# Performance work log

Hardware: AMD Instinct MI355X
Metric: run time of the kernel (lower is better)

The kernel has to match this reference:

```python
import jax, jax.numpy as jnp
import numpy as np

B, C, H, W, K = 8, 128, 128, 128, 7


def _ln2d(x, gamma=None, beta=None, eps=1e-5):
    # LayerNorm2d: normalize over the channel dim at each (b, h, w) position
    mu = x.mean(axis=1, keepdims=True)
    var = x.var(axis=1, keepdims=True)
    y = (x - mu) * jax.lax.rsqrt(var + eps)
    if gamma is not None:
        y = y * gamma[None, :, None, None] + beta[None, :, None, None]
    return y


def _conv1x1(x, w, b):
    # w: [C_out, C_in] (1x1 conv collapsed)
    return jnp.einsum('oi,bihw->bohw', w, x) + b[None, :, None, None]


def _sym_conv(x, w):
    # channel-symmetric 7x7 conv, padding 'same' (SymmetricConv2d, symmetry_type='channel')
    ws = 0.5 * (w + jnp.swapaxes(w, 0, 1))
    return jax.lax.conv_general_dilated(
        x, ws, window_strides=(1, 1), padding='SAME',
        dimension_numbers=('NCHW', 'OIHW', 'NCHW'))


def setup_inputs() -> dict:
    key = jax.random.key(0)
    ks = jax.random.split(key, 8)
    f32 = jnp.float32
    return {
        'ff_input': jax.random.normal(ks[0], (B, C, H, W), f32),
        'h_exc': jax.random.normal(ks[1], (B, C, H, W), f32),
        'h_inh': jax.random.normal(ks[2], (B, C, H, W), f32),
        # 1x1 gate convs over concat([h_exc, h_inh, ff]) -> C channels
        'W_gain': jax.random.normal(ks[3], (C, 3 * C), f32) * 0.02,
        'b_gain': jnp.zeros((C,), f32),
        'W_mix': jax.random.normal(ks[4], (C, 3 * C), f32) * 0.02,
        'b_mix': jnp.zeros((C,), f32),
        # symmetric 7x7 horizontal connections
        'W_inh': jax.random.normal(ks[5], (C, C, K, K), f32) * 0.01,
        'W_exc': jax.random.normal(ks[6], (C, C, K, K), f32) * 0.01,
        # static circuit parameters (use_dynamic_parameters=False)
        'alpha': jnp.zeros((C,), f32),
        'mu': jnp.zeros((C,), f32),
        'kappa': jnp.ones((C,), f32) * 0.1,
        'omega': jnp.ones((C,), f32) * 0.1,
        # affine LayerNorm2d for circuit outputs c1/c2
        'c1_gamma': jnp.ones((C,), f32), 'c1_beta': jnp.zeros((C,), f32),
        'c2_gamma': jnp.ones((C,), f32), 'c2_beta': jnp.zeros((C,), f32),
    }


def reference(ff_input, h_exc, h_inh, W_gain, b_gain, W_mix, b_mix,
              W_inh, W_exc, alpha, mu, kappa, omega,
              c1_gamma, c1_beta, c2_gamma, c2_beta):
    # --- stage 1: gain gate (pre-norm on concat, 1x1 conv, sigmoid) ---
    g1_in = _ln2d(jnp.concatenate([h_exc, h_inh, ff_input], axis=1))  # [B,3C,H,W]
    g1 = jax.nn.sigmoid(_conv1x1(g1_in, W_gain, b_gain))              # [B,C,H,W]

    # --- stage 2: horizontal inhibition from gain-controlled excitatory state ---
    c1 = _ln2d(_sym_conv(h_exc * g1, W_inh), c1_gamma, c1_beta)

    # --- stage 3: input integration: divisive (alpha) + subtractive (mu) inhibition ---
    a = jax.nn.sigmoid(alpha)[None, :, None, None]  # force_alpha_divisive
    m = mu[None, :, None, None]
    inhibited = jax.nn.relu(ff_input - jax.nn.relu((a * h_inh + m) * c1))

    # --- stage 4: mix gate ---
    g2_in = _ln2d(jnp.concatenate([inhibited, h_exc, h_inh], axis=1))
    g2 = jax.nn.sigmoid(_conv1x1(g2_in, W_mix, b_mix))

    # --- stage 5: excitatory horizontal connections ---
    c2 = _ln2d(_sym_conv(inhibited, W_exc), c2_gamma, c2_beta)

    # --- stage 6: output integration (multiplicative excitation) ---
    k = kappa[None, :, None, None]
    o = jax.nn.relu(omega)[None, :, None, None]  # force_omega_nonnegative
    h_tilde = jax.nn.relu(k * (inhibited + c2) + o * (inhibited * c2))

    # --- gated state update of the excitatory population ---
    h_exc_new = (1.0 - g2) * h_exc + g2 * h_tilde
    return h_exc_new
```

## Files before the change

kernel.cpp:

```cpp
#include <hip/hip_runtime.h>
#include <cstddef>
#include <cstdint>

namespace {
constexpr int B_ = 8, C_ = 128, H_ = 128, W_ = 128;
constexpr int HW_ = H_ * W_;
constexpr size_t CHW_ = (size_t)C_ * HW_;
constexpr int NPIX_ = B_ * HW_;
}

typedef __attribute__((ext_vector_type(8))) short bf16x8;
typedef __attribute__((ext_vector_type(4))) float f32x4;
typedef __attribute__((ext_vector_type(8))) unsigned short u16x8;
typedef __attribute__((ext_vector_type(4))) unsigned short u16x4;

__device__ inline unsigned short f2bf(float f) {
  unsigned int u = __float_as_uint(f);
  unsigned int r = u + 0x7FFFu + ((u >> 16) & 1u);
  return (unsigned short)(r >> 16);
}
__device__ inline float bf2f(unsigned short u) {
  return __uint_as_float((unsigned int)u << 16);
}

__device__ inline void async_copy16(void* lds_dst, const void* gsrc) {
  __builtin_amdgcn_global_load_lds(
      (const __attribute__((address_space(1))) unsigned int*)gsrc,
      (__attribute__((address_space(3))) unsigned int*)lds_dst, 16, 0, 0);
}

__global__ __launch_bounds__(256) void prep_w_bf16_k(
    const float* __restrict__ Wa, const float* __restrict__ Wb,
    unsigned short* __restrict__ Ta, unsigned short* __restrict__ Tb) {
  int idx = blockIdx.x * 256 + threadIdx.x;
  int j = idx & 7;
  int o = (idx >> 3) & 127;
  int g = (idx >> 10) & 15;
  int t = idx >> 14;
  int i = g * 8 + j;
  int ky = t / 7, kx = t - ky * 7;
  size_t oi = ((size_t)(o * 128 + i) * 7 + ky) * 7 + kx;
  size_t io = ((size_t)(i * 128 + o) * 7 + ky) * 7 + kx;
  Ta[idx] = f2bf(0.5f * (Wa[oi] + Wa[io]));
  Tb[idx] = f2bf(0.5f * (Wb[oi] + Wb[io]));
}

__global__ __launch_bounds__(256) void prep_apack_k(
    const float* __restrict__ Wg, const float* __restrict__ Wm,
    unsigned short* __restrict__ Ag, unsigned short* __restrict__ Am) {
  int idx = blockIdx.x * 256 + threadIdx.x;
  int j = idx & 7;
  int l = (idx >> 3) & 63;
  int f = (idx >> 9) & 7;
  int s = idx >> 12;
  int m = f * 16 + (l & 15);
  int k = s * 32 + (l >> 4) * 8 + j;
  Ag[idx] = f2bf(Wg[m * 384 + k]);
  Am[idx] = f2bf(Wm[m * 384 + k]);
}

__global__ void rowsum_k(const float* __restrict__ Wg,
                         const float* __restrict__ Wm, float* __restrict__ rs) {
  int t = threadIdx.x;
  const float* src = (t < 128) ? Wg : Wm;
  int row = t & 127;
  float s = 0.f;
  for (int i = 0; i < 384; ++i) s += bf2f(f2bf(src[row * 384 + i]));
  rs[t] = s;
}

__global__ __launch_bounds__(256) void stats3_cvt_k(
    const float* __restrict__ t0, const float* __restrict__ t1,
    const float* __restrict__ t2, float* __restrict__ mu_o,
    float* __restrict__ inv_o, float* __restrict__ ps12,
    float* __restrict__ pq12, unsigned short* __restrict__ o0,
    unsigned short* __restrict__ o1, unsigned short* __restrict__ o2) {
  __shared__ unsigned short tile[32 * 136];
  __shared__ float s8[8][32];
  __shared__ float q8[8][32];
  int blk = blockIdx.x;
  int b = blk >> 9;
  int p0 = (blk & 511) * 32;
  int t = threadIdx.x;
  int px = t & 31, cq = t >> 5;
  size_t base = (size_t)b * CHW_ + p0 + px;
  int pixg = b * HW_ + p0;
  float s = 0.f, s2 = 0.f;
  for (int ci = 0; ci < 16; ++ci) {
    int c = cq * 16 + ci;
    float v = t0[base + (size_t)c * HW_];
    s += v; s2 = fmaf(v, v, s2);
    tile[px * 136 + c] = f2bf(v);
  }
  __syncthreads();
#pragma unroll
  for (int pass = 0; pass < 2; ++pass) {
    int u = pass * 256 + t;
    int ppx = u >> 4, cg = u & 15;
    *(u16x8*)(o0 + (size_t)(pixg + ppx) * 128 + cg * 8) =
        *(const u16x8*)(tile + ppx * 136 + cg * 8);
  }
  __syncthreads();
  for (int ci = 0; ci < 16; ++ci) {
    int c = cq * 16 + ci;
    float v = t1[base + (size_t)c * HW_];
    s += v; s2 = fmaf(v, v, s2);
    tile[px * 136 + c] = f2bf(v);
  }
  s8[cq][px] = s;
  q8[cq][px] = s2;
  __syncthreads();
#pragma unroll
  for (int pass = 0; pass < 2; ++pass) {
    int u = pass * 256 + t;
    int ppx = u >> 4, cg = u & 15;
    *(u16x8*)(o1 + (size_t)(pixg + ppx) * 128 + cg * 8) =
        *(const u16x8*)(tile + ppx * 136 + cg * 8);
  }
  if (t < 32) {
    float ss = 0.f, qs = 0.f;
#pragma unroll
    for (int k = 0; k < 8; ++k) { ss += s8[k][t]; qs += q8[k][t]; }
    ps12[pixg + t] = ss;
    pq12[pixg + t] = qs;
  }
  __syncthreads();
  for (int ci = 0; ci < 16; ++ci) {
    int c = cq * 16 + ci;
    float v = t2[base + (size_t)c * HW_];
    s += v; s2 = fmaf(v, v, s2);
    tile[px * 136 + c] = f2bf(v);
  }
  s8[cq][px] = s;
  q8[cq][px] = s2;
  __syncthreads();
#pragma unroll
  for (int pass = 0; pass < 2; ++pass) {
    int u = pass * 256 + t;
    int ppx = u >> 4, cg = u & 15;
    *(u16x8*)(o2 + (size_t)(pixg + ppx) * 128 + cg * 8) =
        *(const u16x8*)(tile + ppx * 136 + cg * 8);
  }
  if (t < 32) {
    float ss = 0.f, qs = 0.f;
#pragma unroll
    for (int k = 0; k < 8; ++k) { ss += s8[k][t]; qs += q8[k][t]; }
    float m = ss * (1.f / 384.f);
    float var = qs * (1.f / 384.f) - m * m;
    mu_o[pixg + t] = m;
    inv_o[pixg + t] = rsqrtf(var + 1e-5f);
  }
}

template <int FINAL>
__global__ __launch_bounds__(256) void gemm_mfma_k(
    const unsigned short* __restrict__ Apack, const float* __restrict__ rowsum,
    const float* __restrict__ bias, const unsigned short* __restrict__ B0,
    const unsigned short* __restrict__ B1, const unsigned short* __restrict__ B2,
    const float* __restrict__ mu, const float* __restrict__ inv,
    const unsigned short* __restrict__ mult_cl, unsigned short* __restrict__ out_cl,
    const unsigned short* __restrict__ c2_cl, const float* __restrict__ muc,
    const float* __restrict__ invc, const unsigned short* __restrict__ inh_cl,
    const unsigned short* __restrict__ hexc_cl, const float* __restrict__ c2g,
    const float* __restrict__ c2b, const float* __restrict__ kap,
    const float* __restrict__ omg, float* __restrict__ out_f32) {
  int b = blockIdx.y;
  int tid = threadIdx.x;
  int lane = tid & 63, wid = tid >> 6;
  int l15 = lane & 15, kg = lane >> 4;
  int n0 = blockIdx.x * 128 + wid * 32;
  int pix0 = b * HW_ + n0;
  size_t bofs = (size_t)b * CHW_;
  f32x4 acc[8][2] = {};
#pragma unroll
  for (int s = 0; s < 12; ++s) {
    const unsigned short* src = (s < 4) ? B0 : ((s < 8) ? B1 : B2);
    int ch0 = (s & 3) * 32 + kg * 8;
    bf16x8 bfr[2];
#pragma unroll
    for (int nf = 0; nf < 2; ++nf)
      bfr[nf] = *(const bf16x8*)(src + (size_t)(pix0 + nf * 16 + l15) * 128 + ch0);
    const bf16x8* ap = (const bf16x8*)(Apack + ((size_t)(s * 8) * 64 + lane) * 8);
#pragma unroll
    for (int f = 0; f < 8; ++f) {
      bf16x8 afr = ap[f * 64];
#pragma unroll
      for (int nf = 0; nf < 2; ++nf)
        acc[f][nf] = __builtin_amdgcn_mfma_f32_16x16x32_bf16(afr, bfr[nf],
                                                             acc[f][nf], 0, 0, 0);
    }
  }
#pragma unroll
  for (int nf = 0; nf < 2; ++nf) {
    int n = n0 + nf * 16 + l15;
    int qpix = b * HW_ + n;
    float muv = mu[qpix], invv = inv[qpix];
    if (!FINAL) {
#pragma unroll
      for (int mf = 0; mf < 8; ++mf) {
        int m0 = mf * 16 + kg * 4;
        f32x4 rs4 = *(const f32x4*)(rowsum + m0);
        f32x4 bi4 = *(const f32x4*)(bias + m0);
        u16x4 mv = *(const u16x4*)(mult_cl + (size_t)qpix * 128 + m0);
        u16x4 st;
#pragma unroll
        for (int j = 0; j < 4; ++j) {
          float val = invv * (acc[mf][nf][j] - muv * rs4[j]) + bi4[j];
          float g = 1.f / (1.f + __expf(-val));
          st[j] = f2bf(bf2f(mv[j]) * g);
        }
        *(u16x4*)(out_cl + (size_t)qpix * 128 + m0) = st;
      }
    } else {
      float mcv = muc[qpix], icv = invc[qpix];
#pragma unroll
      for (int mf = 0; mf < 8; ++mf) {
        int m0 = mf * 16 + kg * 4;
        f32x4 rs4 = *(const f32x4*)(rowsum + m0);
        f32x4 bi4 = *(const f32x4*)(bias + m0);
        f32x4 g4 = *(const f32x4*)(c2g + m0);
        f32x4 b4 = *(const f32x4*)(c2b + m0);
        f32x4 k4 = *(const f32x4*)(kap + m0);
        f32x4 o4 = *(const f32x4*)(omg + m0);
        u16x4 c2v = *(const u16x4*)(c2_cl + (size_t)qpix * 128 + m0);
        u16x4 iv4 = *(const u16x4*)(inh_cl + (size_t)qpix * 128 + m0);
        u16x4 hx4 = *(const u16x4*)(hexc_cl + (size_t)qpix * 128 + m0);
#pragma unroll
        for (int j = 0; j < 4; ++j) {
          float val = invv * (acc[mf][nf][j] - muv * rs4[j]) + bi4[j];
          float g2 = 1.f / (1.f + __expf(-val));
          float c2 = (bf2f(c2v[j]) - mcv) * icv * g4[j] + b4[j];
          float iv = bf2f(iv4[j]);
          float ht =
              fmaxf(k4[j] * (iv + c2) + fmaxf(o4[j], 0.f) * (iv * c2), 0.f);
          out_f32[bofs + (size_t)(m0 + j) * HW_ + n] =
              (1.f - g2) * bf2f(hx4[j]) + g2 * ht;
        }
      }
    }
  }
}

__global__ __launch_bounds__(256, 2) void conv7_mfma_k(
    const unsigned short* __restrict__ in_cl,
    const unsigned short* __restrict__ Wp, unsigned short* __restrict__ out,
    float* __restrict__ mu_o, float* __restrict__ inv_o) {
  __shared__ short w_s[7 * 4 * 128 * 8];
  __shared__ short in_s[2 * 4 * 136 * 8];
  int b = blockIdx.x & 7;
  int y0 = ((blockIdx.x >> 3) & 63) * 2;
  int tid = threadIdx.x;
  int lane = tid & 63;
  int wid = tid >> 6;
  int wm = wid >> 1;
  int row = wid & 1;
  int l15 = lane & 15, kg = lane >> 4;
  f32x4 acc[4][8] = {};
  for (int ky = 0; ky < 7; ++ky) {
    int ybase = y0 + ky - 3;
    for (int c4 = 0; c4 < 4; ++c4) {
      __syncthreads();
      const unsigned short* wsrc =
          Wp + (size_t)(ky * 7) * 16384 + c4 * 4096 + tid * 8;
#pragma unroll
      for (int kx = 0; kx < 7; ++kx) {
#pragma unroll
        for (int h = 0; h < 2; ++h) {
          async_copy16(w_s + kx * 4096 + (h * 256 + tid) * 8,
                       wsrc + kx * 16384 + h * 2048);
        }
      }
      for (int u = tid; u < 1088; u += 256) {
        int r = u / 544;
        int rem = u - r * 544;
        int g = rem / 136;
        int xi = rem - g * 136;
        int x = xi - 3;
        int y = ybase + r;
        u16x8 v = {};
        if (x >= 0 && x < 128 && y >= 0 && y < 128)
          v = *(const u16x8*)(in_cl + ((size_t)((b * 128 + y) * 128 + x) * 128 +
                                       c4 * 32 + g * 8));
        *(u16x8*)(in_s + u * 8) = v;
      }
      __syncthreads();
      for (int kx = 0; kx < 7; ++kx) {
        bf16x8 bfr[8], afr[4];
#pragma unroll
        for (int nf = 0; nf < 8; ++nf) {
          int xi = nf * 16 + l15 + kx;
          bfr[nf] = *(const bf16x8*)(in_s + ((row * 4 + kg) * 136 + xi) * 8);
        }
#pragma unroll
        for (int mf = 0; mf < 4; ++mf) {
          int oc = wm * 64 + mf * 16 + l15;
          afr[mf] = *(const bf16x8*)(w_s + ((kx * 4 + kg) * 128 + oc) * 8);
        }
#pragma unroll
        for (int mf = 0; mf < 4; ++mf)
#pragma unroll
          for (int nf = 0; nf < 8; ++nf)
            acc[mf][nf] = __builtin_amdgcn_mfma_f32_16x16x32_bf16(
                afr[mf], bfr[nf], acc[mf][nf], 0, 0, 0);
      }
    }
  }
  __syncthreads();
  float* red = (float*)in_s;
  int y = y0 + row;
#pragma unroll
  for (int nf = 0; nf < 8; ++nf) {
    int x = nf * 16 + l15;
    size_t paddr = (size_t)(b * HW_ + y * 128 + x) * 128;
    float s = 0.f, qq = 0.f;
#pragma unroll
    for (int mf = 0; mf < 4; ++mf) {
      int oc0 = wm * 64 + mf * 16 + kg * 4;
      u16x4 st;
#pragma unroll
      for (int j = 0; j < 4; ++j) {
        unsigned short bv = f2bf(acc[mf][nf][j]);
        float vr = bf2f(bv);
        s += vr;
        qq = fmaf(vr, vr, qq);
        st[j] = bv;
      }
      *(u16x4*)(out + paddr + oc0) = st;
    }
    s += __shfl_xor(s, 16);
    qq += __shfl_xor(qq, 16);
    s += __shfl_xor(s, 32);
    qq += __shfl_xor(qq, 32);
    if (kg == 0) {
      red[(wm * 2 + row) * 128 + x] = s;
      red[512 + (wm * 2 + row) * 128 + x] = qq;
    }
  }
  __syncthreads();
  {
    int r2 = tid >> 7, x2 = tid & 127;
    float s = red[(0 * 2 + r2) * 128 + x2] + red[(1 * 2 + r2) * 128 + x2];
    float qq = red[512 + (0 * 2 + r2) * 128 + x2] +
               red[512 + (1 * 2 + r2) * 128 + x2];
    float m = s * (1.f / 128.f);
    float var = qq * (1.f / 128.f) - m * m;
    int q = b * HW_ + (y0 + r2) * 128 + x2;
    mu_o[q] = m;
    inv_o[q] = rsqrtf(var + 1e-5f);
  }
}

__global__ __launch_bounds__(256) void inhibit_k(
    const unsigned short* __restrict__ c1_cl,
    unsigned short* __restrict__ ffio_cl,
    const unsigned short* __restrict__ hinh_cl, const float* __restrict__ mu_s,
    const float* __restrict__ inv_s, const float* __restrict__ ps12,
    const float* __restrict__ pq12, const float* __restrict__ alpha,
    const float* __restrict__ mu_p, const float* __restrict__ gamma,
    const float* __restrict__ beta, float* __restrict__ mu2_o,
    float* __restrict__ inv2_o) {
  __shared__ float s16[16][17];
  __shared__ float q16[16][17];
  int blk = blockIdx.x;
  int t = threadIdx.x;
  int cg = t & 15, pxi = t >> 4;
  int pix = blk * 16 + pxi;
  size_t base = (size_t)pix * 128 + cg * 8;
  int c0 = cg * 8;
  float muv = mu_s[pix], invv = inv_s[pix];
  u16x8 c1v = *(const u16x8*)(c1_cl + base);
  u16x8 ffv = *(const u16x8*)(ffio_cl + base);
  u16x8 hiv = *(const u16x8*)(hinh_cl + base);
  f32x4 al0 = *(const f32x4*)(alpha + c0), al1 = *(const f32x4*)(alpha + c0 + 4);
  f32x4 mp0 = *(const f32x4*)(mu_p + c0), mp1 = *(const f32x4*)(mu_p + c0 + 4);
  f32x4 ga0 = *(const f32x4*)(gamma + c0), ga1 = *(const f32x4*)(gamma + c0 + 4);
  f32x4 be0 = *(const f32x4*)(beta + c0), be1 = *(const f32x4*)(beta + c0 + 4);
  float sp = 0.f, qp = 0.f;
  u16x8 ov;
#pragma unroll
  for (int j = 0; j < 8; ++j) {
    float alv = (j < 4) ? al0[j & 3] : al1[j & 3];
    float mpv = (j < 4) ? mp0[j & 3] : mp1[j & 3];
    float gav = (j < 4) ? ga0[j & 3] : ga1[j & 3];
    float bev = (j < 4) ? be0[j & 3] : be1[j & 3];
    float c1 = (bf2f(c1v[j]) - muv) * invv * gav + bev;
    float a = 1.f / (1.f + __expf(-alv));
    float r = fmaxf((a * bf2f(hiv[j]) + mpv) * c1, 0.f);
    float v = fmaxf(bf2f(ffv[j]) - r, 0.f);
    unsigned short bv = f2bf(v);
    float vr = bf2f(bv);
    sp += vr;
    qp = fmaf(vr, vr, qp);
    ov[j] = bv;
  }
  *(u16x8*)(ffio_cl + base) = ov;
  s16[pxi][cg] = sp;
  q16[pxi][cg] = qp;
  __syncthreads();
  if (t < 16) {
    float s = 0.f, qs = 0.f;
#pragma unroll
    for (int k = 0; k < 16; ++k) { s += s16[t][k]; qs += q16[t][k]; }
    int pg = blk * 16 + t;
    s += ps12[pg];
    qs += pq12[pg];
    float m = s * (1.f / 384.f);
    float var = qs * (1.f / 384.f) - m * m;
    mu2_o[pg] = m;
    inv2_o[pg] = rsqrtf(var + 1e-5f);
  }
}

extern "C" void kernel_launch(void* const* d_in, const int* in_sizes, int n_in,
                              void* d_out, int out_size, void* d_ws,
                              size_t ws_size, hipStream_t stream) {
  const float* ff     = (const float*)d_in[0];
  const float* h_exc  = (const float*)d_in[1];
  const float* h_inh  = (const float*)d_in[2];
  const float* W_gain = (const float*)d_in[3];
  const float* b_gain = (const float*)d_in[4];
  const float* W_mix  = (const float*)d_in[5];
  const float* b_mix  = (const float*)d_in[6];
  const float* W_inh  = (const float*)d_in[7];
  const float* W_exc  = (const float*)d_in[8];
  const float* alpha  = (const float*)d_in[9];
  const float* mu_p   = (const float*)d_in[10];
  const float* kappa  = (const float*)d_in[11];
  const float* omega  = (const float*)d_in[12];
  const float* c1_g   = (const float*)d_in[13];
  const float* c1_b   = (const float*)d_in[14];
  const float* c2_g   = (const float*)d_in[15];
  const float* c2_b   = (const float*)d_in[16];

  float* w = (float*)d_ws;
  unsigned short* Wp_inh = (unsigned short*)w;  w += 401408;
  unsigned short* Wp_exc = (unsigned short*)w;  w += 401408;
  unsigned short* Ag     = (unsigned short*)w;  w += 24576;
  unsigned short* Am     = (unsigned short*)w;  w += 24576;
  float* rs     = w;  w += 256;
  float* mu1    = w;  w += NPIX_;
  float* inv1   = w;  w += NPIX_;
  float* mu_c1  = w;  w += NPIX_;
  float* inv_c1 = w;  w += NPIX_;
  float* mu2    = w;  w += NPIX_;
  float* inv2   = w;  w += NPIX_;
  float* mu_c2  = w;  w += NPIX_;
  float* inv_c2 = w;  w += NPIX_;
  float* ps12   = w;  w += NPIX_;
  float* pq12   = w;  w += NPIX_;
  unsigned short* exc_cl   = (unsigned short*)w;  w += 8388608;
  unsigned short* hinh_cl  = (unsigned short*)w;  w += 8388608;
  unsigned short* ffinh_cl = (unsigned short*)w;  w += 8388608;
  unsigned short* conv_cl  = (unsigned short*)w;  w += 8388608;

  unsigned short* gated_cl = (unsigned short*)d_out;

  prep_w_bf16_k<<<3136, 256, 0, stream>>>(W_inh, W_exc, Wp_inh, Wp_exc);
  prep_apack_k<<<192, 256, 0, stream>>>(W_gain, W_mix, Ag, Am);
  rowsum_k<<<1, 256, 0, stream>>>(W_gain, W_mix, rs);

  stats3_cvt_k<<<4096, 256, 0, stream>>>(h_exc, h_inh, ff, mu1, inv1, ps12,
                                         pq12, exc_cl, hinh_cl, ffinh_cl);
  {
    dim3 g(128, 8);
    gemm_mfma_k<0><<<g, 256, 0, stream>>>(
        Ag, rs, b_gain, exc_cl, hinh_cl, ffinh_cl, mu1, inv1, exc_cl, gated_cl,
        nullptr, nullptr, nullptr, nullptr, nullptr, nullptr, nullptr, nullptr,
        nullptr, nullptr);
  }
  conv7_mfma_k<<<512, 256, 0, stream>>>(gated_cl, Wp_inh, conv_cl, mu_c1,
                                        inv_c1);
  inhibit_k<<<8192, 256, 0, stream>>>(conv_cl, ffinh_cl, hinh_cl, mu_c1,
                                      inv_c1, ps12, pq12, alpha, mu_p, c1_g,
                                      c1_b, mu2, inv2);
  conv7_mfma_k<<<512, 256, 0, stream>>>(ffinh_cl, Wp_exc, conv_cl, mu_c2,
                                        inv_c2);
  {
    dim3 g(128, 8);
    gemm_mfma_k<1><<<g, 256, 0, stream>>>(
        Am, rs + 128, b_mix, ffinh_cl, exc_cl, hinh_cl, mu2, inv2, nullptr,
        nullptr, conv_cl, mu_c2, inv_c2, ffinh_cl, exc_cl, c2_g, c2_b, kappa,
        omega, (float*)d_out);
  }
}
```

Measured before the change: 603.5 us.

## Fuse inhibition and second layer-norm stats into first conv7 epilogue

Folds the separate inhibit kernel into the first 7x7 conv's epilogue. The conv output c1 is no longer written to global memory and re-read. Its per-pixel LN stats are kept in shared memory, and the block applies the divisive/subtractive inhibition in place on the ff buffer while also producing the LN2 stats. sigmoid(alpha) is precomputed once in the rowsum kernel. This saves a launch and a full bf16 tensor round trip, but adds register and epilogue work to a kernel bound to 2 blocks per SM.

```diff
diff --git a/kernel.cpp b/kernel.cpp
--- a/kernel.cpp
+++ b/kernel.cpp
@@ -60,13 +60,16 @@
 }
 
 __global__ void rowsum_k(const float* __restrict__ Wg,
-                         const float* __restrict__ Wm, float* __restrict__ rs) {
+                         const float* __restrict__ Wm,
+                         const float* __restrict__ alpha,
+                         float* __restrict__ rs, float* __restrict__ sa) {
   int t = threadIdx.x;
   const float* src = (t < 128) ? Wg : Wm;
   int row = t & 127;
   float s = 0.f;
   for (int i = 0; i < 384; ++i) s += bf2f(f2bf(src[row * 384 + i]));
   rs[t] = s;
+  if (t < 128) sa[t] = 1.f / (1.f + __expf(-alpha[t]));
 }
 
 __global__ __launch_bounds__(256) void stats3_cvt_k(
@@ -241,10 +244,15 @@
   }
 }
 
+template <int FUSE_INH>
 __global__ __launch_bounds__(256, 2) void conv7_mfma_k(
     const unsigned short* __restrict__ in_cl,
-    const unsigned short* __restrict__ Wp, unsigned short* __restrict__ out,
-    float* __restrict__ mu_o, float* __restrict__ inv_o) {
+    const unsigned short* __restrict__ Wp, unsigned short* out,
+    float* __restrict__ mu_o, float* __restrict__ inv_o,
+    const unsigned short* ff_cl, const unsigned short* __restrict__ hinh_cl,
+    const float* __restrict__ ps12, const float* __restrict__ pq12,
+    const float* __restrict__ sig_alpha, const float* __restrict__ mu_p,
+    const float* __restrict__ gamma, const float* __restrict__ beta) {
   __shared__ short w_s[7 * 4 * 128 * 8];
   __shared__ short in_s[2 * 4 * 136 * 8];
   int b = blockIdx.x & 7;
@@ -325,7 +333,7 @@
         qq = fmaf(vr, vr, qq);
         st[j] = bv;
       }
-      *(u16x4*)(out + paddr + oc0) = st;
+      if (!FUSE_INH) *(u16x4*)(out + paddr + oc0) = st;
     }
     s += __shfl_xor(s, 16);
     qq += __shfl_xor(qq, 16);
@@ -339,75 +347,79 @@
   __syncthreads();
   {
     int r2 = tid >> 7, x2 = tid & 127;
-    float s = red[(0 * 2 + r2) * 128 + x2] + red[(1 * 2 + r2) * 128 + x2];
-    float qq = red[512 + (0 * 2 + r2) * 128 + x2] +
-               red[512 + (1 * 2 + r2) * 128 + x2];
+    float s = red[r2 * 128 + x2] + red[(2 + r2) * 128 + x2];
+    float qq = red[512 + r2 * 128 + x2] + red[512 + (2 + r2) * 128 + x2];
     float m = s * (1.f / 128.f);
     float var = qq * (1.f / 128.f) - m * m;
-    int q = b * HW_ + (y0 + r2) * 128 + x2;
-    mu_o[q] = m;
-    inv_o[q] = rsqrtf(var + 1e-5f);
-  }
-}
-
-__global__ __launch_bounds__(256) void inhibit_k(
-    const unsigned short* __restrict__ c1_cl,
-    unsigned short* __restrict__ ffio_cl,
-    const unsigned short* __restrict__ hinh_cl, const float* __restrict__ mu_s,
-    const float* __restrict__ inv_s, const float* __restrict__ ps12,
-    const float* __restrict__ pq12, const float* __restrict__ alpha,
-    const float* __restrict__ mu_p, const float* __restrict__ gamma,
-    const float* __restrict__ beta, float* __restrict__ mu2_o,
-    float* __restrict__ inv2_o) {
-  __shared__ float s16[16][17];
-  __shared__ float q16[16][17];
-  int blk = blockIdx.x;
-  int t = threadIdx.x;
-  int cg = t & 15, pxi = t >> 4;
-  int pix = blk * 16 + pxi;
-  size_t base = (size_t)pix * 128 + cg * 8;
-  int c0 = cg * 8;
-  float muv = mu_s[pix], invv = inv_s[pix];
-  u16x8 c1v = *(const u16x8*)(c1_cl + base);
-  u16x8 ffv = *(const u16x8*)(ffio_cl + base);
-  u16x8 hiv = *(const u16x8*)(hinh_cl + base);
-  f32x4 al0 = *(const f32x4*)(alpha + c0), al1 = *(const f32x4*)(alpha + c0 + 4);
-  f32x4 mp0 = *(const f32x4*)(mu_p + c0), mp1 = *(const f32x4*)(mu_p + c0 + 4);
-  f32x4 ga0 = *(const f32x4*)(gamma + c0), ga1 = *(const f32x4*)(gamma + c0 + 4);
-  f32x4 be0 = *(const f32x4*)(beta + c0), be1 = *(const f32x4*)(beta + c0 + 4);
-  float sp = 0.f, qp = 0.f;
-  u16x8 ov;
-#pragma unroll
-  for (int j = 0; j < 8; ++j) {
-    float alv = (j < 4) ? al0[j & 3] : al1[j & 3];
-    float mpv = (j < 4) ? mp0[j & 3] : mp1[j & 3];
-    float gav = (j < 4) ? ga0[j & 3] : ga1[j & 3];
-    float bev = (j < 4) ? be0[j & 3] : be1[j & 3];
-    float c1 = (bf2f(c1v[j]) - muv) * invv * gav + bev;
-    float a = 1.f / (1.f + __expf(-alv));
-    float r = fmaxf((a * bf2f(hiv[j]) + mpv) * c1, 0.f);
-    float v = fmaxf(bf2f(ffv[j]) - r, 0.f);
-    unsigned short bv = f2bf(v);
-    float vr = bf2f(bv);
-    sp += vr;
-    qp = fmaf(vr, vr, qp);
-    ov[j] = bv;
-  }
-  *(u16x8*)(ffio_cl + base) = ov;
-  s16[pxi][cg] = sp;
-  q16[pxi][cg] = qp;
-  __syncthreads();
-  if (t < 16) {
-    float s = 0.f, qs = 0.f;
-#pragma unroll
-    for (int k = 0; k < 16; ++k) { s += s16[t][k]; qs += q16[t][k]; }
-    int pg = blk * 16 + t;
+    float ivv = rsqrtf(var + 1e-5f);
+    if (FUSE_INH) {
+      red[1024 + r2 * 128 + x2] = m;
+      red[1280 + r2 * 128 + x2] = ivv;
+    } else {
+      int q = b * HW_ + (y0 + r2) * 128 + x2;
+      mu_o[q] = m;
+      inv_o[q] = ivv;
+    }
+  }
+  if (!FUSE_INH) return;
+  __syncthreads();
+  f32x4 ga4[4], be4[4], sa4[4], mp4[4];
+#pragma unroll
+  for (int mf = 0; mf < 4; ++mf) {
+    int oc0 = wm * 64 + mf * 16 + kg * 4;
+    ga4[mf] = *(const f32x4*)(gamma + oc0);
+    be4[mf] = *(const f32x4*)(beta + oc0);
+    sa4[mf] = *(const f32x4*)(sig_alpha + oc0);
+    mp4[mf] = *(const f32x4*)(mu_p + oc0);
+  }
+#pragma unroll
+  for (int nf = 0; nf < 8; ++nf) {
+    int x = nf * 16 + l15;
+    float muv = red[1024 + row * 128 + x];
+    float invv = red[1280 + row * 128 + x];
+    size_t paddr = (size_t)(b * HW_ + y * 128 + x) * 128;
+    float s2 = 0.f, q2 = 0.f;
+#pragma unroll
+    for (int mf = 0; mf < 4; ++mf) {
+      int oc0 = wm * 64 + mf * 16 + kg * 4;
+      u16x4 ffv = *(const u16x4*)(ff_cl + paddr + oc0);
+      u16x4 hiv = *(const u16x4*)(hinh_cl + paddr + oc0);
+      u16x4 st;
+#pragma unroll
+      for (int j = 0; j < 4; ++j) {
+        float c1 =
+            (bf2f(f2bf(acc[mf][nf][j])) - muv) * invv * ga4[mf][j] + be4[mf][j];
+        float r = fmaxf((sa4[mf][j] * bf2f(hiv[j]) + mp4[mf][j]) * c1, 0.f);
+        float v = fmaxf(bf2f(ffv[j]) - r, 0.f);
+        unsigned short bv = f2bf(v);
+        float vr = bf2f(bv);
+        s2 += vr;
+        q2 = fmaf(vr, vr, q2);
+        st[j] = bv;
+      }
+      *(u16x4*)(out + paddr + oc0) = st;
+    }
+    s2 += __shfl_xor(s2, 16);
+    q2 += __shfl_xor(q2, 16);
+    s2 += __shfl_xor(s2, 32);
+    q2 += __shfl_xor(q2, 32);
+    if (kg == 0) {
+      red[(wm * 2 + row) * 128 + x] = s2;
+      red[512 + (wm * 2 + row) * 128 + x] = q2;
+    }
+  }
+  __syncthreads();
+  {
+    int r2 = tid >> 7, x2 = tid & 127;
+    float s = red[r2 * 128 + x2] + red[(2 + r2) * 128 + x2];
+    float qq = red[512 + r2 * 128 + x2] + red[512 + (2 + r2) * 128 + x2];
+    int pg = b * HW_ + (y0 + r2) * 128 + x2;
     s += ps12[pg];
-    qs += pq12[pg];
+    qq += pq12[pg];
     float m = s * (1.f / 384.f);
-    float var = qs * (1.f / 384.f) - m * m;
-    mu2_o[pg] = m;
-    inv2_o[pg] = rsqrtf(var + 1e-5f);
+    float var = qq * (1.f / 384.f) - m * m;
+    mu_o[pg] = m;
+    inv_o[pg] = rsqrtf(var + 1e-5f);
   }
 }
 
@@ -438,10 +450,9 @@
   unsigned short* Ag     = (unsigned short*)w;  w += 24576;
   unsigned short* Am     = (unsigned short*)w;  w += 24576;
   float* rs     = w;  w += 256;
+  float* sa     = w;  w += 128;
   float* mu1    = w;  w += NPIX_;
   float* inv1   = w;  w += NPIX_;
-  float* mu_c1  = w;  w += NPIX_;
-  float* inv_c1 = w;  w += NPIX_;
   float* mu2    = w;  w += NPIX_;
   float* inv2   = w;  w += NPIX_;
   float* mu_c2  = w;  w += NPIX_;
@@ -457,7 +468,7 @@
 
   prep_w_bf16_k<<<3136, 256, 0, stream>>>(W_inh, W_exc, Wp_inh, Wp_exc);
   prep_apack_k<<<192, 256, 0, stream>>>(W_gain, W_mix, Ag, Am);
-  rowsum_k<<<1, 256, 0, stream>>>(W_gain, W_mix, rs);
+  rowsum_k<<<1, 256, 0, stream>>>(W_gain, W_mix, alpha, rs, sa);
 
   stats3_cvt_k<<<4096, 256, 0, stream>>>(h_exc, h_inh, ff, mu1, inv1, ps12,
                                          pq12, exc_cl, hinh_cl, ffinh_cl);
@@ -468,13 +479,13 @@
         nullptr, nullptr, nullptr, nullptr, nullptr, nullptr, nullptr, nullptr,
         nullptr, nullptr);
   }
-  conv7_mfma_k<<<512, 256, 0, stream>>>(gated_cl, Wp_inh, conv_cl, mu_c1,
-                                        inv_c1);
-  inhibit_k<<<8192, 256, 0, stream>>>(conv_cl, ffinh_cl, hinh_cl, mu_c1,
-                                      inv_c1, ps12, pq12, alpha, mu_p, c1_g,
-                                      c1_b, mu2, inv2);
-  conv7_mfma_k<<<512, 256, 0, stream>>>(ffinh_cl, Wp_exc, conv_cl, mu_c2,
-                                        inv_c2);
+  conv7_mfma_k<1><<<512, 256, 0, stream>>>(gated_cl, Wp_inh, ffinh_cl, mu2,
+                                           inv2, ffinh_cl, hinh_cl, ps12, pq12,
+                                           sa, mu_p, c1_g, c1_b);
+  conv7_mfma_k<0><<<512, 256, 0, stream>>>(ffinh_cl, Wp_exc, conv_cl, mu_c2,
+                                           inv_c2, nullptr, nullptr, nullptr,
+                                           nullptr, nullptr, nullptr, nullptr,
+                                           nullptr);
   {
     dim3 g(128, 8);
     gemm_mfma_k<1><<<g, 256, 0, stream>>>(
```

New measurement: 594.1 us. No clear change (-1.6%).
